# Kernel tuning notes

Measured on AMD Instinct MI355X. Metric: run time of the kernel, lower is better.

The kernel has to match this reference:

```python
import jax, jax.numpy as jnp
import numpy as np

T, B, I, H, L = 512, 64, 512, 1024, 2

def setup_inputs() -> dict:
    key = jax.random.key(0)
    ks = jax.random.split(key, 9)
    stdv = 1.0 / np.sqrt(H)
    u = lambda k, shape: jax.random.uniform(k, shape, jnp.float32, -stdv, stdv)
    return {
        "x": jax.random.normal(ks[0], (T, B, I), jnp.float32),
        "w_ih0": u(ks[1], (4 * H, I)),
        "w_hh0": u(ks[2], (4 * H, H)),
        "b_ih0": u(ks[3], (4 * H,)),
        "b_hh0": u(ks[4], (4 * H,)),
        "w_ih1": u(ks[5], (4 * H, H)),
        "w_hh1": u(ks[6], (4 * H, H)),
        "b_ih1": u(ks[7], (4 * H,)),
        "b_hh1": u(ks[8], (4 * H,)),
    }

def _lstm_cell(x, h, c, w_ih, w_hh, b_ih, b_hh):
    # gates: [B, 4H]
    gates = x @ w_ih.T + b_ih + h @ w_hh.T + b_hh
    i, f, g, o = jnp.split(gates, 4, axis=1)
    c_new = jax.nn.sigmoid(f) * c + jax.nn.sigmoid(i) * jnp.tanh(g)
    h_new = jax.nn.sigmoid(o) * jnp.tanh(c_new)
    return h_new, c_new

def reference(x, w_ih0, w_hh0, b_ih0, b_hh0, w_ih1, w_hh1, b_ih1, b_hh1):
    layers = [(w_ih0, w_hh0, b_ih0, b_hh0), (w_ih1, w_hh1, b_ih1, b_hh1)]
    h0 = jnp.zeros((L, B, H), x.dtype)
    c0 = jnp.zeros((L, B, H), x.dtype)

    def step(carry, x_t):
        h, c = carry
        inp = x_t
        hs, cs = [], []
        for l, (w_ih, w_hh, b_ih, b_hh) in enumerate(layers):
            h_new, c_new = _lstm_cell(inp, h[l], c[l], w_ih, w_hh, b_ih, b_hh)
            hs.append(h_new)
            cs.append(c_new)
            inp = h_new
        return (jnp.stack(hs), jnp.stack(cs)), inp

    (h_f, c_f), out = jax.lax.scan(step, (h0, c0), x)
    return out, (h_f, c_f)
```

## Files before the change

### kernel.cpp

```cpp
#include <hip/hip_runtime.h>

#define TT 512
#define BB 64
#define II 512
#define HH 1024
#define NBLK 256
#define NTHR 512
#define NCTR 32
#define CSTRIDE 32

typedef short bf16x8 __attribute__((ext_vector_type(8)));
typedef float f32x4 __attribute__((ext_vector_type(4)));
typedef int   i32x4 __attribute__((ext_vector_type(4)));

struct Params {
  const unsigned short* xb;
  unsigned short* h0;
  unsigned short* h1;
  unsigned int* ctr;
  const float* wih0; const float* whh0; const float* bih0; const float* bhh0;
  const float* wih1; const float* whh1; const float* bih1; const float* bhh1;
  float* out;
};

__device__ __forceinline__ unsigned short f2bf(float f) {
  unsigned int u = __float_as_uint(f);
  u += 0x7fffu + ((u >> 16) & 1u);
  return (unsigned short)(u >> 16);
}

__device__ __forceinline__ bf16x8 ld_bypass(const unsigned short* p) {
  i32x4 r;
  asm volatile("global_load_dwordx4 %0, %1, off sc0 sc1" : "=v"(r) : "v"(p));
  return __builtin_bit_cast(bf16x8, r);
}

__device__ __forceinline__ void st_bypass_b128(unsigned short* p, i32x4 v) {
  asm volatile("global_store_dwordx4 %0, %1, off sc0 sc1" :: "v"(p), "v"(v) : "memory");
}

__global__ void cvt_kernel(const float* __restrict__ x, unsigned short* __restrict__ xb, int n8) {
  int i = blockIdx.x * blockDim.x + threadIdx.x;
  int stride = gridDim.x * blockDim.x;
  for (; i < n8; i += stride) {
    const float4* p = (const float4*)(x) + (size_t)i * 2;
    float4 a = p[0], b = p[1];
    bf16x8 v;
    v[0] = (short)f2bf(a.x); v[1] = (short)f2bf(a.y); v[2] = (short)f2bf(a.z); v[3] = (short)f2bf(a.w);
    v[4] = (short)f2bf(b.x); v[5] = (short)f2bf(b.y); v[6] = (short)f2bf(b.z); v[7] = (short)f2bf(b.w);
    ((bf16x8*)xb)[i] = v;
  }
}

template <int LAYER>
__device__ void body(const Params& P, float (*pbuf)[64][36], float (*cb)[16],
                     unsigned short (*hbuf)[16]) {
  constexpr int K   = (LAYER == 0) ? (II + HH) : (2 * HH);
  constexpr int KSL = K / (8 * 32);
  constexpr int NG  = KSL / 2;
  constexpr int KIH = (LAYER == 0) ? II : HH;

  const int tid  = threadIdx.x;
  const int lane = tid & 63;
  const int kh   = tid >> 6;
  const int lbid = blockIdx.x & 127;
  const int mh   = lbid >> 6;
  const int ns   = lbid & 63;
  const int l15  = lane & 15;
  const int lk8  = (lane >> 4) * 8;

  const float* wih = (LAYER == 0) ? P.wih0 : P.wih1;
  const float* whh = (LAYER == 0) ? P.whh0 : P.whh1;

  bf16x8 wf[4][KSL];
  #pragma unroll
  for (int nt = 0; nt < 4; ++nt) {
    const int row = nt * HH + ns * 16 + l15;
    #pragma unroll
    for (int ks = 0; ks < KSL; ++ks) {
      int k = kh * (KSL * 32) + ks * 32 + lk8;
      const float* src = (k < KIH) ? (wih + (size_t)row * KIH + k)
                                   : (whh + (size_t)row * HH + (k - KIH));
      const float4* p4 = (const float4*)src;
      float4 a = p4[0], b = p4[1];
      bf16x8 v;
      v[0] = (short)f2bf(a.x); v[1] = (short)f2bf(a.y); v[2] = (short)f2bf(a.z); v[3] = (short)f2bf(a.w);
      v[4] = (short)f2bf(b.x); v[5] = (short)f2bf(b.y); v[6] = (short)f2bf(b.z); v[7] = (short)f2bf(b.w);
      wf[nt][ks] = v;
    }
  }

  float bv[4];
  {
    const float* bi = (LAYER == 0) ? P.bih0 : P.bih1;
    const float* bh = (LAYER == 0) ? P.bhh0 : P.bhh1;
    int unit = ns * 16 + (tid & 15);
    #pragma unroll
    for (int g = 0; g < 4; ++g) bv[g] = bi[g * HH + unit] + bh[g * HH + unit];
  }

  if (tid < 128) {
    int q = tid >> 4, j = tid & 15;
    #pragma unroll
    for (int r = 0; r < 4; ++r) cb[q * 4 + r][j] = 0.f;
  }

  const size_t BH  = (size_t)BB * HH;
  const size_t TBH = (size_t)TT * BH;

  #pragma unroll 1
  for (int p = 0; p <= TT; ++p) {
    const int t = (LAYER == 0) ? p : p - 1;
    const bool active = (LAYER == 0) ? (p < TT) : (p >= 1);

    f32x4 acc[2][4];
    float hv[4];
    if (active) {
      #pragma unroll
      for (int mt = 0; mt < 2; ++mt)
        #pragma unroll
        for (int nt = 0; nt < 4; ++nt) acc[mt][nt] = f32x4{0.f, 0.f, 0.f, 0.f};

      const unsigned short* h0prev = P.h0 + (size_t)((t + 1) & 1) * BH;
      const unsigned short* h0cur  = P.h0 + (size_t)(t & 1) * BH;
      const unsigned short* h1prev = P.h1 + (size_t)((t + 1) & 1) * BH;

      bf16x8 af[2][2][2];

      auto issue_group = [&](int g, int pp) {
        #pragma unroll
        for (int ksb = 0; ksb < 2; ++ksb) {
          const int ks = g * 2 + ksb;
          const int k  = kh * (KSL * 32) + ks * 32 + lk8;
          #pragma unroll
          for (int mt = 0; mt < 2; ++mt) {
            const int m = mh * 32 + mt * 16 + l15;
            const unsigned short* src;
            if (LAYER == 0) {
              src = (k < II) ? (P.xb + ((size_t)t * BB + m) * II + k)
                             : (h0prev + (size_t)m * HH + (k - II));
            } else {
              src = (k < HH) ? (h0cur + (size_t)m * HH + k)
                             : (h1prev + (size_t)m * HH + (k - HH));
            }
            af[pp][ksb][mt] = ld_bypass(src);
          }
        }
      };

      issue_group(0, 0);
      issue_group(1, 1);
      #pragma unroll
      for (int g = 0; g < NG; ++g) {
        if (g < NG - 1) asm volatile("s_waitcnt vmcnt(4)" ::: "memory");
        else            asm volatile("s_waitcnt vmcnt(0)" ::: "memory");
        __builtin_amdgcn_sched_barrier(0);
        #pragma unroll
        for (int ksb = 0; ksb < 2; ++ksb) {
          const int ks = g * 2 + ksb;
          #pragma unroll
          for (int mt = 0; mt < 2; ++mt)
            #pragma unroll
            for (int nt = 0; nt < 4; ++nt)
              acc[mt][nt] = __builtin_amdgcn_mfma_f32_16x16x32_bf16(af[g & 1][ksb][mt], wf[nt][ks], acc[mt][nt], 0, 0, 0);
        }
        if (g + 2 < NG) issue_group(g + 2, g & 1);
      }

      if (kh >= 4) {
        #pragma unroll
        for (int mt = 0; mt < 2; ++mt)
          #pragma unroll
          for (int nt = 0; nt < 4; ++nt) {
            int col = nt * 16 + l15;
            int mb  = mt * 16 + (lane >> 4) * 4;
            *(f32x4*)&pbuf[kh - 4][col][mb] = acc[mt][nt];
          }
      }
    }
    __syncthreads();
    if (active && kh < 4) {
      #pragma unroll
      for (int mt = 0; mt < 2; ++mt)
        #pragma unroll
        for (int nt = 0; nt < 4; ++nt) {
          int col = nt * 16 + l15;
          int mb  = mt * 16 + (lane >> 4) * 4;
          f32x4 v = *(const f32x4*)&pbuf[kh][col][mb];
          acc[mt][nt] += v;
          *(f32x4*)&pbuf[kh][col][mb] = acc[mt][nt];
        }
    }
    __syncthreads();
    if (active && tid < 128) {
      int q = tid >> 4, j = tid & 15;
      f32x4 gv[4];
      #pragma unroll
      for (int g = 0; g < 4; ++g) {
        int col = g * 16 + j;
        f32x4 s = *(const f32x4*)&pbuf[0][col][q * 4];
        #pragma unroll
        for (int w = 1; w < 4; ++w) s += *(const f32x4*)&pbuf[w][col][q * 4];
        gv[g] = s;
      }
      #pragma unroll
      for (int r = 0; r < 4; ++r) {
        int m = q * 4 + r;
        float iv = 1.f / (1.f + __expf(-(gv[0][r] + bv[0])));
        float fv = 1.f / (1.f + __expf(-(gv[1][r] + bv[1])));
        float gg = tanhf(gv[2][r] + bv[2]);
        float ov = 1.f / (1.f + __expf(-(gv[3][r] + bv[3])));
        float c = fv * cb[m][j] + iv * gg;
        cb[m][j] = c;
        float h = ov * tanhf(c);
        hv[r] = h;
        hbuf[m][j] = f2bf(h);
      }
    }
    __syncthreads();
    if (tid < 64) {
      if (active) {
        int row  = tid >> 1;
        int half = tid & 1;
        i32x4 v = *(const i32x4*)&hbuf[row][half * 8];
        unsigned short* dst = ((LAYER == 0) ? P.h0 : P.h1) +
            (size_t)(t & 1) * BH + (size_t)(mh * 32 + row) * HH + ns * 16 + half * 8;
        st_bypass_b128(dst, v);
      }
      asm volatile("s_waitcnt vmcnt(0)" ::: "memory");
      if (tid == 0)
        __hip_atomic_fetch_add(&P.ctr[(blockIdx.x & (NCTR - 1)) * CSTRIDE], 1u,
                               __ATOMIC_RELAXED, __HIP_MEMORY_SCOPE_AGENT);
    }
    if (active && tid < 128) {
      int q = tid >> 4, j = tid & 15;
      #pragma unroll
      for (int r = 0; r < 4; ++r) {
        int mg = mh * 32 + q * 4 + r;
        int unit = ns * 16 + j;
        if (LAYER == 0) {
          if (t == TT - 1) P.out[TBH + (size_t)mg * HH + unit] = hv[r];
        } else {
          P.out[(size_t)t * BH + (size_t)mg * HH + unit] = hv[r];
          if (t == TT - 1) P.out[TBH + BH + (size_t)mg * HH + unit] = hv[r];
        }
      }
    }
    if (tid < NCTR) {
      unsigned int target = (unsigned)(NBLK / NCTR) * (unsigned)(p + 1);
      while (__hip_atomic_load(&P.ctr[tid * CSTRIDE], __ATOMIC_RELAXED,
                               __HIP_MEMORY_SCOPE_AGENT) < target) {
        __builtin_amdgcn_s_sleep(1);
      }
    }
    __syncthreads();
  }

  if (tid < 128) {
    int q = tid >> 4, j = tid & 15;
    #pragma unroll
    for (int r = 0; r < 4; ++r) {
      int m = q * 4 + r;
      int mg = mh * 32 + m;
      int unit = ns * 16 + j;
      P.out[TBH + (size_t)(2 + LAYER) * BH + (size_t)mg * HH + unit] = cb[m][j];
    }
  }
}

__global__ void __launch_bounds__(NTHR, 1) lstm_kernel(Params P) {
  __shared__ float pbuf[4][64][36];
  __shared__ float cb[32][16];
  __shared__ unsigned short hbuf[32][16];
  if (blockIdx.x < 128) body<0>(P, pbuf, cb, hbuf);
  else                  body<1>(P, pbuf, cb, hbuf);
}

extern "C" void kernel_launch(void* const* d_in, const int* in_sizes, int n_in,
                              void* d_out, int out_size, void* d_ws, size_t ws_size,
                              hipStream_t stream) {
  const float* x = (const float*)d_in[0];
  Params P;
  P.wih0 = (const float*)d_in[1];
  P.whh0 = (const float*)d_in[2];
  P.bih0 = (const float*)d_in[3];
  P.bhh0 = (const float*)d_in[4];
  P.wih1 = (const float*)d_in[5];
  P.whh1 = (const float*)d_in[6];
  P.bih1 = (const float*)d_in[7];
  P.bhh1 = (const float*)d_in[8];
  P.out  = (float*)d_out;

  char* ws = (char*)d_ws;
  P.ctr = (unsigned int*)ws;
  P.xb  = (const unsigned short*)(ws + 8192);
  unsigned short* xb_w = (unsigned short*)(ws + 8192);
  P.h0  = (unsigned short*)(ws + 8192 + (size_t)TT * BB * II * 2);
  P.h1  = P.h0 + (size_t)2 * BB * HH;

  hipMemsetAsync((void*)P.ctr, 0, 8192, stream);
  hipMemsetAsync((void*)P.h0, 0, (size_t)4 * BB * HH * sizeof(unsigned short), stream);

  int n8 = TT * BB * II / 8;
  cvt_kernel<<<2048, 256, 0, stream>>>(x, xb_w, n8);

  void* args[] = { &P };
  hipLaunchCooperativeKernel((void*)lstm_kernel, dim3(NBLK), dim3(NTHR), args, 0, stream);
}
```

Before: 4.456 ms.

## Replace global barrier with per-set dependency flags and 4-deep h ring buffers

Replaces the grid-wide atomic counter barrier at the end of each timestep with per-block flag stores, grouped into sets by layer and batch half. Each block polls only the producer sets it actually needs before the step. The hidden-state buffers grow from double to quadruple buffering so layer 0 can run up to two steps ahead of layer 1 without overwriting data still being read. This removes the all-block synchronization stall and lets the two layers pipeline loosely, at the cost of more polling traffic and subtler memory-ordering assumptions.

```diff
diff --git a/kernel.cpp b/kernel.cpp
--- a/kernel.cpp
+++ b/kernel.cpp
@@ -6,8 +6,7 @@
 #define HH 1024
 #define NBLK 256
 #define NTHR 512
-#define NCTR 32
-#define CSTRIDE 32
+#define FSTRIDE 128
 
 typedef short bf16x8 __attribute__((ext_vector_type(8)));
 typedef float f32x4 __attribute__((ext_vector_type(4)));
@@ -17,7 +16,7 @@
   const unsigned short* xb;
   unsigned short* h0;
   unsigned short* h1;
-  unsigned int* ctr;
+  unsigned int* flags;
   const float* wih0; const float* whh0; const float* bih0; const float* bhh0;
   const float* wih1; const float* whh1; const float* bih1; const float* bhh1;
   float* out;
@@ -34,9 +33,16 @@
   asm volatile("global_load_dwordx4 %0, %1, off sc0 sc1" : "=v"(r) : "v"(p));
   return __builtin_bit_cast(bf16x8, r);
 }
-
 __device__ __forceinline__ void st_bypass_b128(unsigned short* p, i32x4 v) {
   asm volatile("global_store_dwordx4 %0, %1, off sc0 sc1" :: "v"(p), "v"(v) : "memory");
+}
+__device__ __forceinline__ void st_bypass_u32(unsigned int* p, unsigned int v) {
+  asm volatile("global_store_dword %0, %1, off sc0 sc1" :: "v"(p), "v"(v) : "memory");
+}
+
+__device__ __forceinline__ void poll_set(const unsigned int* f, int lane, unsigned int tgt) {
+  while (__hip_atomic_load(&f[lane], __ATOMIC_RELAXED, __HIP_MEMORY_SCOPE_AGENT) < tgt)
+    __builtin_amdgcn_s_sleep(4);
 }
 
 __global__ void cvt_kernel(const float* __restrict__ x, unsigned short* __restrict__ xb, int n8) {
@@ -68,6 +74,10 @@
   const int ns   = lbid & 63;
   const int l15  = lane & 15;
   const int lk8  = (lane >> 4) * 8;
+
+  const int setL0 = mh;
+  const int setL1 = 2 + mh;
+  const int fset  = LAYER * 2 + mh;
 
   const float* wih = (LAYER == 0) ? P.wih0 : P.wih1;
   const float* whh = (LAYER == 0) ? P.whh0 : P.whh1;
@@ -113,6 +123,18 @@
     const int t = (LAYER == 0) ? p : p - 1;
     const bool active = (LAYER == 0) ? (p < TT) : (p >= 1);
 
+    if (kh == 0 && p >= 1) {
+      poll_set(P.flags + (size_t)setL0 * FSTRIDE, lane, (unsigned)p);
+    }
+    if (kh == 1) {
+      if (LAYER == 0) {
+        if (p >= 3) poll_set(P.flags + (size_t)setL1 * FSTRIDE, lane, (unsigned)(p - 2));
+      } else {
+        if (p >= 1) poll_set(P.flags + (size_t)setL1 * FSTRIDE, lane, (unsigned)p);
+      }
+    }
+    __syncthreads();
+
     f32x4 acc[2][4];
     float hv[4];
     if (active) {
@@ -121,9 +143,9 @@
         #pragma unroll
         for (int nt = 0; nt < 4; ++nt) acc[mt][nt] = f32x4{0.f, 0.f, 0.f, 0.f};
 
-      const unsigned short* h0prev = P.h0 + (size_t)((t + 1) & 1) * BH;
-      const unsigned short* h0cur  = P.h0 + (size_t)(t & 1) * BH;
-      const unsigned short* h1prev = P.h1 + (size_t)((t + 1) & 1) * BH;
+      const unsigned short* h0prev = P.h0 + (size_t)((t - 1) & 3) * BH;
+      const unsigned short* h0cur  = P.h0 + (size_t)(t & 3) * BH;
+      const unsigned short* h1prev = P.h1 + (size_t)((t - 1) & 3) * BH;
 
       bf16x8 af[2][2][2];
 
@@ -224,13 +246,12 @@
         int half = tid & 1;
         i32x4 v = *(const i32x4*)&hbuf[row][half * 8];
         unsigned short* dst = ((LAYER == 0) ? P.h0 : P.h1) +
-            (size_t)(t & 1) * BH + (size_t)(mh * 32 + row) * HH + ns * 16 + half * 8;
+            (size_t)(t & 3) * BH + (size_t)(mh * 32 + row) * HH + ns * 16 + half * 8;
         st_bypass_b128(dst, v);
       }
       asm volatile("s_waitcnt vmcnt(0)" ::: "memory");
       if (tid == 0)
-        __hip_atomic_fetch_add(&P.ctr[(blockIdx.x & (NCTR - 1)) * CSTRIDE], 1u,
-                               __ATOMIC_RELAXED, __HIP_MEMORY_SCOPE_AGENT);
+        st_bypass_u32(P.flags + (size_t)fset * FSTRIDE + ns, (unsigned)(p + 1));
     }
     if (active && tid < 128) {
       int q = tid >> 4, j = tid & 15;
@@ -246,14 +267,6 @@
         }
       }
     }
-    if (tid < NCTR) {
-      unsigned int target = (unsigned)(NBLK / NCTR) * (unsigned)(p + 1);
-      while (__hip_atomic_load(&P.ctr[tid * CSTRIDE], __ATOMIC_RELAXED,
-                               __HIP_MEMORY_SCOPE_AGENT) < target) {
-        __builtin_amdgcn_s_sleep(1);
-      }
-    }
-    __syncthreads();
   }
 
   if (tid < 128) {
@@ -292,14 +305,14 @@
   P.out  = (float*)d_out;
 
   char* ws = (char*)d_ws;
-  P.ctr = (unsigned int*)ws;
+  P.flags = (unsigned int*)ws;
   P.xb  = (const unsigned short*)(ws + 8192);
   unsigned short* xb_w = (unsigned short*)(ws + 8192);
   P.h0  = (unsigned short*)(ws + 8192 + (size_t)TT * BB * II * 2);
-  P.h1  = P.h0 + (size_t)2 * BB * HH;
-
-  hipMemsetAsync((void*)P.ctr, 0, 8192, stream);
-  hipMemsetAsync((void*)P.h0, 0, (size_t)4 * BB * HH * sizeof(unsigned short), stream);
+  P.h1  = P.h0 + (size_t)4 * BB * HH;
+
+  hipMemsetAsync((void*)P.flags, 0, 8192, stream);
+  hipMemsetAsync((void*)P.h0, 0, (size_t)8 * BB * HH * sizeof(unsigned short), stream);
 
   int n8 = TT * BB * II / 8;
   cvt_kernel<<<2048, 256, 0, stream>>>(x, xb_w, n8);
```

Result: slower. 5.010 ms (+12.4%).
